# Kernel tuning notes

Measured on AMD Instinct MI355X. Metric: run time of the kernel, lower is better.

## Reference

```python
import jax, jax.numpy as jnp
import numpy as np

THRESHOLD = 0.0  # default float threshold, non-learned path
SURROGATE_TAU = 0.1

@jax.custom_vjp
def jumprelu(x):
    # Forward: hard threshold x * 1[x > THRESHOLD]
    return x * (x > THRESHOLD).astype(x.dtype)

def _jumprelu_fwd(x):
    return jumprelu(x), x

def _jumprelu_bwd(x, g):
    # Smooth surrogate gradient of x * sigmoid(x/tau)
    tau = SURROGATE_TAU
    sig = jax.nn.sigmoid(x / tau)
    surrogate = sig + x * sig * (1.0 - sig) / tau
    return (g * surrogate,)

jumprelu.defvjp(_jumprelu_fwd, _jumprelu_bwd)

NUM_TRANSFORMS = 64
D_MODEL = 2048
RANK = 32
BATCH = 2048

def setup_inputs() -> dict:
    key = jax.random.key(0)
    kx, kv, ku, ke = jax.random.split(key, 4)
    scale = (1.0 / (D_MODEL * RANK)) ** 0.25
    x = jax.random.normal(kx, (BATCH, D_MODEL), dtype=jnp.float32)
    V = jax.random.normal(kv, (NUM_TRANSFORMS, RANK, D_MODEL), dtype=jnp.float32) * scale
    U = jax.random.normal(ku, (NUM_TRANSFORMS, D_MODEL, RANK), dtype=jnp.float32) * scale
    encoder = jax.random.normal(ke, (NUM_TRANSFORMS, D_MODEL), dtype=jnp.float32)
    encoder = encoder / jnp.linalg.norm(encoder, axis=1, keepdims=True)
    bias = jnp.full((NUM_TRANSFORMS,), -1.0, dtype=jnp.float32)
    return {"x": x, "V": V, "U": U, "encoder": encoder, "bias": bias}

def reference(x, V, U, encoder, bias):
    # pre_acts: (batch, num_transforms)
    pre_acts = x @ encoder.T - bias
    gate = jumprelu(pre_acts)
    # Vx: (n, b, r); UVx: (n, b, d)
    Vx = jnp.einsum('nrd,bd->nbr', V, x)
    UVx = jnp.einsum('ndr,nbr->nbd', U, Vx)
    gated = UVx * gate.T[:, :, None]
    output = gated.sum(axis=0)  # (batch, d_model)
    u_norms = jnp.linalg.norm(U.reshape(U.shape[0], -1), axis=1)
    v_norms = jnp.linalg.norm(V.reshape(V.shape[0], -1), axis=1)
    frobenius_norms = u_norms * v_norms / (D_MODEL * RANK) ** 0.5
    return (output, gate, frobenius_norms)
```

## Files before the change

kernel.cpp:

```cpp
#include <hip/hip_runtime.h>


#define D_MODEL 2048
#define BATCH   2048
#define NT      64
#define RANK    32

typedef __attribute__((ext_vector_type(8))) __bf16 bf16x8;
typedef __attribute__((ext_vector_type(4))) float  f32x4;

__device__ __forceinline__ unsigned short f2bf(float f) {
  unsigned int u = __builtin_bit_cast(unsigned int, f);
  u += 0x7FFFu + ((u >> 16) & 1u);
  return (unsigned short)(u >> 16);
}

__device__ __forceinline__ void gload_lds16(const void* g, void* l) {
  __builtin_amdgcn_global_load_lds(
      (const __attribute__((address_space(1))) unsigned int*)g,
      (__attribute__((address_space(3))) unsigned int*)l,
      16, 0, 0);
}


__device__ __forceinline__ void block_reduce_store(float ss, float* dst, int slot) {
  __shared__ float red[256];
  int t = threadIdx.x;
  red[t] = ss;
  __syncthreads();
  for (int s = 128; s > 0; s >>= 1) {
    if (t < s) red[t] += red[t + s];
    __syncthreads();
  }
  if (t == 0) dst[slot] = red[0];
}

__global__ void k_prep(const float4* __restrict__ x, const float4* __restrict__ enc,
                       const float4* __restrict__ V, const float4* __restrict__ U,
                       ushort4* __restrict__ xb, ushort4* __restrict__ encb,
                       ushort4* __restrict__ Vb, unsigned short* __restrict__ Ut,
                       float* __restrict__ partV, float* __restrict__ partU) {
  int bid = blockIdx.x, t = threadIdx.x;
  if (bid < 1024) {
#pragma unroll
    for (int it = 0; it < 4; ++it) {
      int i = bid * 1024 + it * 256 + t;
      float4 v = x[i];
      ushort4 o;
      o.x = f2bf(v.x); o.y = f2bf(v.y); o.z = f2bf(v.z); o.w = f2bf(v.w);
      xb[i] = o;
    }
  } else if (bid < 1152) {
    int i = (bid - 1024) * 256 + t;
    float4 v = enc[i];
    ushort4 o;
    o.x = f2bf(v.x); o.y = f2bf(v.y); o.z = f2bf(v.z); o.w = f2bf(v.w);
    encb[i] = o;
  } else if (bid < 1408) {
    int b = bid - 1152;
    size_t base4 = (size_t)b * 4096;
    float ss = 0.f;
    for (int it = 0; it < 16; ++it) {
      size_t idx = base4 + t + it * 256;
      float4 v = V[idx];
      ss += v.x * v.x + v.y * v.y + v.z * v.z + v.w * v.w;
      ushort4 o;
      o.x = f2bf(v.x); o.y = f2bf(v.y); o.z = f2bf(v.z); o.w = f2bf(v.w);
      Vb[idx] = o;
    }
    block_reduce_store(ss, partV, b);
  } else {
    int b = bid - 1408;
    int n = b >> 2;
    size_t base4 = (size_t)b * 4096;
    float ss = 0.f;
    for (int it = 0; it < 16; ++it) {
      size_t idx4 = base4 + t + it * 256;
      float4 v = U[idx4];
      ss += v.x * v.x + v.y * v.y + v.z * v.z + v.w * v.w;
      size_t e = idx4 * 4 - (size_t)n * (D_MODEL * RANK);
      int dcol = (int)(e >> 5);
      int r = (int)(e & 31);
      ushort4 o;
      o.x = f2bf(v.x); o.y = f2bf(v.y); o.z = f2bf(v.z); o.w = f2bf(v.w);
      *(ushort4*)(Ut + (size_t)dcol * 2048 + n * 32 + r) = o;
    }
    block_reduce_store(ss, partU, b);
  }
}

__global__ void k_gate_reduce(const float* __restrict__ part, const float* __restrict__ bias,
                              float* __restrict__ gate,
                              const float* __restrict__ pU, const float* __restrict__ pV,
                              float* __restrict__ frob) {
  int t = threadIdx.x;
  if (blockIdx.x == 0 && t < NT) {
    float su = pU[4 * t] + pU[4 * t + 1] + pU[4 * t + 2] + pU[4 * t + 3];
    float sv = pV[4 * t] + pV[4 * t + 1] + pV[4 * t + 2] + pV[4 * t + 3];
    frob[t] = sqrtf(su) * sqrtf(sv) * (1.0f / 256.0f);
  }
#pragma unroll
  for (int u = 0; u < 4; ++u) {
    int idx = blockIdx.x * 1024 + u * 256 + t;
    float s = 0.f;
#pragma unroll
    for (int z = 0; z < 8; ++z) s += part[(size_t)z * (BATCH * NT) + idx];
    float pre = s - bias[idx & (NT - 1)];
    gate[idx] = pre > 0.f ? pre : 0.f;
  }
}

template <int WGM, int WGN, int MI, int NJ, int EPI, int SWZ>
__global__ __launch_bounds__(WGM * WGN * 64, 2)
void gemm_bt(const unsigned short* __restrict__ A,
             const unsigned short* __restrict__ Bt,
             const float* __restrict__ aux,
             unsigned short* __restrict__ outB,
             float* __restrict__ outF, int K, int klen) {
  constexpr int VW = WGM * WGN;
  constexpr int BM = WGM * MI * 16;
  constexpr int BN = WGN * NJ * 16;
  constexpr int GA = (BM / 8) / VW;
  constexpr int GB = (BN / 8) / VW;
  constexpr int HBUF = (BM + BN) * 64;
  __shared__ __align__(16) unsigned short smem[2 * HBUF];

  const int tid = threadIdx.x;
  const int w = tid >> 6;
  const int lane = tid & 63;
  const int quad = lane >> 4;
  const int l15 = lane & 15;
  const int wm = w % WGM;
  const int wn = w / WGM;

  int blockM, blockN, kbeg;
  if constexpr (SWZ) {
    const int lin = blockIdx.x;
    const int xcd = lin & 7;
    const int i = lin >> 3;
    blockM = (xcd & 3) * 4 + (i & 3);
    blockN = (xcd >> 2) * 8 + (i >> 2);
    kbeg = 0;
  } else {
    blockN = blockIdx.x;
    blockM = blockIdx.y;
    kbeg = blockIdx.z * klen;
  }

  const int lrow = lane >> 3;
  const int lq = (lane & 7) ^ lrow;
  const unsigned short* Ag = A + (size_t)(blockM * BM + lrow) * K + kbeg + lq * 8;
  const unsigned short* Bg = Bt + (size_t)(blockN * BN + lrow) * K + kbeg + lq * 8;

  const int pcs = (quad ^ (lane & 7)) * 16;
  const int rfA = wm * MI * 16 + l15;
  const int rfB = wn * NJ * 16 + l15;

  f32x4 acc[MI][NJ];
  const f32x4 z = {0.f, 0.f, 0.f, 0.f};
#pragma unroll
  for (int i = 0; i < MI; ++i)
#pragma unroll
    for (int j = 0; j < NJ; ++j) acc[i][j] = z;

  auto stage = [&](int buf, int k0) {
    unsigned short* As = smem + buf * HBUF;
    unsigned short* Bs = As + BM * 64;
#pragma unroll
    for (int j = 0; j < GA; ++j)
      gload_lds16(Ag + (size_t)((j * VW + w) * 8) * K + k0,
                  (char*)As + (j * VW + w) * 1024);
#pragma unroll
    for (int j = 0; j < GB; ++j)
      gload_lds16(Bg + (size_t)((j * VW + w) * 8) * K + k0,
                  (char*)Bs + (j * VW + w) * 1024);
  };

  stage(0, 0);
  __syncthreads();

  const int nt = klen / 64;
  int cur = 0;
  for (int t = 0; t < nt; ++t) {
    if (t + 1 < nt) stage(cur ^ 1, (t + 1) * 64);
    const unsigned short* As = smem + cur * HBUF;
    const unsigned short* Bs = As + BM * 64;
#pragma unroll
    for (int s = 0; s < 2; ++s) {
      bf16x8 af[MI], bfr[NJ];
#pragma unroll
      for (int i = 0; i < MI; ++i)
        af[i] = *(const bf16x8*)((const char*)As + (rfA + i * 16) * 128 + (pcs ^ (s << 6)));
#pragma unroll
      for (int j = 0; j < NJ; ++j)
        bfr[j] = *(const bf16x8*)((const char*)Bs + (rfB + j * 16) * 128 + (pcs ^ (s << 6)));
#pragma unroll
      for (int i = 0; i < MI; ++i)
#pragma unroll
        for (int j = 0; j < NJ; ++j)
          acc[i][j] = __builtin_amdgcn_mfma_f32_16x16x32_bf16(af[i], bfr[j], acc[i][j], 0, 0, 0);
    }
    __syncthreads();
    cur ^= 1;
  }

  const int row0 = blockM * BM + wm * MI * 16 + quad * 4;
  const int col0 = blockN * BN + wn * NJ * 16 + l15;
#pragma unroll
  for (int i = 0; i < MI; ++i) {
#pragma unroll
    for (int j = 0; j < NJ; ++j) {
      const int col = col0 + j * 16;
#pragma unroll
      for (int t = 0; t < 4; ++t) {
        const int row = row0 + i * 16 + t;
        float v = acc[i][j][t];
        if constexpr (EPI == 0) {
          float g = aux[(size_t)row * NT + (col >> 5)];
          outB[(size_t)row * 2048 + col] = f2bf(v * g);
        } else if constexpr (EPI == 1) {
          outF[(size_t)row * 2048 + col] = v;
        } else {
          outF[(size_t)blockIdx.z * (BATCH * NT) + (size_t)row * NT + col] = v;
        }
      }
    }
  }
}


extern "C" void kernel_launch(void* const* d_in, const int* in_sizes, int n_in,
                              void* d_out, int out_size, void* d_ws, size_t ws_size,
                              hipStream_t stream) {
  const float* x    = (const float*)d_in[0];
  const float* V    = (const float*)d_in[1];
  const float* U    = (const float*)d_in[2];
  const float* enc  = (const float*)d_in[3];
  const float* bias = (const float*)d_in[4];

  float* out  = (float*)d_out;
  float* gate = out + (size_t)BATCH * D_MODEL;
  float* frob = gate + (size_t)BATCH * NT;

  char* ws = (char*)d_ws;
  unsigned short* xb   = (unsigned short*)(ws);
  unsigned short* Vb   = (unsigned short*)(ws + (8u << 20));
  unsigned short* Ut   = (unsigned short*)(ws + (16u << 20));
  unsigned short* Yg   = (unsigned short*)(ws + (24u << 20));
  float* gatePart      = (float*)Yg;
  unsigned short* encb = (unsigned short*)(ws + (32u << 20));
  float* partU = (float*)(ws + (32u << 20) + 262144);
  float* partV = partU + 256;

  k_prep<<<1664, 256, 0, stream>>>((const float4*)x, (const float4*)enc,
                                   (const float4*)V, (const float4*)U,
                                   (ushort4*)xb, (ushort4*)encb, (ushort4*)Vb, Ut,
                                   partV, partU);

  gemm_bt<4, 1, 2, 4, 3, 0><<<dim3(1, 16, 8), 256, 0, stream>>>(
      xb, encb, nullptr, nullptr, gatePart, D_MODEL, 256);
  k_gate_reduce<<<128, 256, 0, stream>>>(gatePart, bias, gate, partU, partV, frob);

  gemm_bt<2, 4, 4, 2, 0, 1><<<dim3(256, 1, 1), 512, 0, stream>>>(
      xb, Vb, gate, Yg, nullptr, D_MODEL, D_MODEL);

  gemm_bt<2, 4, 4, 2, 1, 1><<<dim3(256, 1, 1), 512, 0, stream>>>(
      Yg, Ut, nullptr, nullptr, out, D_MODEL, D_MODEL);
}
```

Baseline: 156.5 us.

## Double GEMM K-tile to 128 with new LDS swizzle; widen U transpose stores

The bf16 MFMA GEMM now stages K tiles of 128 instead of 64, with a new 16-way XOR swizzle for the direct global-to-LDS loads and fragment reads. This halves the number of k-loop iterations and barriers, at the cost of double the shared memory per block, which may lower occupancy. Separately, the U conversion/transpose loop processes two float4 per iteration and writes 16-byte bf16 stores to cut store instruction count.

```diff
diff --git a/kernel.cpp b/kernel.cpp
--- a/kernel.cpp
+++ b/kernel.cpp
@@ -8,6 +8,7 @@
 
 typedef __attribute__((ext_vector_type(8))) __bf16 bf16x8;
 typedef __attribute__((ext_vector_type(4))) float  f32x4;
+typedef __attribute__((ext_vector_type(8))) unsigned short ushort8;
 
 __device__ __forceinline__ unsigned short f2bf(float f) {
   unsigned int u = __builtin_bit_cast(unsigned int, f);
@@ -74,16 +75,20 @@
     int n = b >> 2;
     size_t base4 = (size_t)b * 4096;
     float ss = 0.f;
-    for (int it = 0; it < 16; ++it) {
-      size_t idx4 = base4 + t + it * 256;
-      float4 v = U[idx4];
-      ss += v.x * v.x + v.y * v.y + v.z * v.z + v.w * v.w;
+    for (int it = 0; it < 8; ++it) {
+      size_t i2 = (size_t)(it * 256 + t) * 2;
+      size_t idx4 = base4 + i2;
+      float4 v0 = U[idx4];
+      float4 v1 = U[idx4 + 1];
+      ss += v0.x * v0.x + v0.y * v0.y + v0.z * v0.z + v0.w * v0.w;
+      ss += v1.x * v1.x + v1.y * v1.y + v1.z * v1.z + v1.w * v1.w;
       size_t e = idx4 * 4 - (size_t)n * (D_MODEL * RANK);
       int dcol = (int)(e >> 5);
       int r = (int)(e & 31);
-      ushort4 o;
-      o.x = f2bf(v.x); o.y = f2bf(v.y); o.z = f2bf(v.z); o.w = f2bf(v.w);
-      *(ushort4*)(Ut + (size_t)dcol * 2048 + n * 32 + r) = o;
+      ushort8 o;
+      o[0] = f2bf(v0.x); o[1] = f2bf(v0.y); o[2] = f2bf(v0.z); o[3] = f2bf(v0.w);
+      o[4] = f2bf(v1.x); o[5] = f2bf(v1.y); o[6] = f2bf(v1.z); o[7] = f2bf(v1.w);
+      *(ushort8*)(Ut + (size_t)dcol * 2048 + n * 32 + r) = o;
     }
     block_reduce_store(ss, partU, b);
   }
@@ -120,9 +125,10 @@
   constexpr int VW = WGM * WGN;
   constexpr int BM = WGM * MI * 16;
   constexpr int BN = WGN * NJ * 16;
-  constexpr int GA = (BM / 8) / VW;
-  constexpr int GB = (BN / 8) / VW;
-  constexpr int HBUF = (BM + BN) * 64;
+  constexpr int BK = 128;
+  constexpr int GA = BM / (4 * VW);
+  constexpr int GB = BN / (4 * VW);
+  constexpr int HBUF = (BM + BN) * BK;
   __shared__ __align__(16) unsigned short smem[2 * HBUF];
 
   const int tid = threadIdx.x;
@@ -147,12 +153,12 @@
     kbeg = blockIdx.z * klen;
   }
 
-  const int lrow = lane >> 3;
-  const int lq = (lane & 7) ^ lrow;
-  const unsigned short* Ag = A + (size_t)(blockM * BM + lrow) * K + kbeg + lq * 8;
-  const unsigned short* Bg = Bt + (size_t)(blockN * BN + lrow) * K + kbeg + lq * 8;
-
-  const int pcs = (quad ^ (lane & 7)) * 16;
+  const int lrow4 = lane >> 4;
+  const int key = ((w & 3) << 2) | lrow4;
+  const int lq = l15 ^ key;
+  const unsigned short* Ag = A + (size_t)(blockM * BM + w * 4 + lrow4) * K + kbeg + lq * 8;
+  const unsigned short* Bg = Bt + (size_t)(blockN * BN + w * 4 + lrow4) * K + kbeg + lq * 8;
+
   const int rfA = wm * MI * 16 + l15;
   const int rfB = wn * NJ * 16 + l15;
 
@@ -165,35 +171,37 @@
 
   auto stage = [&](int buf, int k0) {
     unsigned short* As = smem + buf * HBUF;
-    unsigned short* Bs = As + BM * 64;
+    unsigned short* Bs = As + BM * BK;
 #pragma unroll
     for (int j = 0; j < GA; ++j)
-      gload_lds16(Ag + (size_t)((j * VW + w) * 8) * K + k0,
+      gload_lds16(Ag + (size_t)(j * VW * 4) * K + k0,
                   (char*)As + (j * VW + w) * 1024);
 #pragma unroll
     for (int j = 0; j < GB; ++j)
-      gload_lds16(Bg + (size_t)((j * VW + w) * 8) * K + k0,
+      gload_lds16(Bg + (size_t)(j * VW * 4) * K + k0,
                   (char*)Bs + (j * VW + w) * 1024);
   };
 
   stage(0, 0);
   __syncthreads();
 
-  const int nt = klen / 64;
+  const int nt = klen / BK;
   int cur = 0;
   for (int t = 0; t < nt; ++t) {
-    if (t + 1 < nt) stage(cur ^ 1, (t + 1) * 64);
+    if (t + 1 < nt) stage(cur ^ 1, (t + 1) * BK);
     const unsigned short* As = smem + cur * HBUF;
-    const unsigned short* Bs = As + BM * 64;
-#pragma unroll
-    for (int s = 0; s < 2; ++s) {
+    const unsigned short* Bs = As + BM * BK;
+#pragma unroll
+    for (int s = 0; s < 4; ++s) {
       bf16x8 af[MI], bfr[NJ];
 #pragma unroll
       for (int i = 0; i < MI; ++i)
-        af[i] = *(const bf16x8*)((const char*)As + (rfA + i * 16) * 128 + (pcs ^ (s << 6)));
+        af[i] = *(const bf16x8*)((const char*)As + (rfA + i * 16) * 256 +
+                                 (((s * 4 + quad) ^ l15) << 4));
 #pragma unroll
       for (int j = 0; j < NJ; ++j)
-        bfr[j] = *(const bf16x8*)((const char*)Bs + (rfB + j * 16) * 128 + (pcs ^ (s << 6)));
+        bfr[j] = *(const bf16x8*)((const char*)Bs + (rfB + j * 16) * 256 +
+                                  (((s * 4 + quad) ^ l15) << 4));
 #pragma unroll
       for (int i = 0; i < MI; ++i)
 #pragma unroll
```

Result: faster. 147.6 us (-5.7%).
